# Optimization experiments

Hardware: AMD Instinct MI355X
Metric: run time of the kernel (lower is better)

Reference implementation:

```python
import jax, jax.numpy as jnp
import numpy as np

N_NODES = 50000
N_EDGES = 800000
D_IN = 64
D_OUT = 64


def setup_inputs() -> dict:
    key = jax.random.key(0)
    k1, k2, k3, k4 = jax.random.split(key, 4)
    x = jax.random.normal(k1, (N_NODES, D_IN), dtype=jnp.float32)
    edge_index = jax.random.randint(k2, (2, N_EDGES), 0, N_NODES, dtype=jnp.int64)
    W = jax.random.normal(k3, (D_IN, D_OUT), dtype=jnp.float32) * (1.0 / np.sqrt(D_IN))
    b = jax.random.normal(k4, (D_OUT,), dtype=jnp.float32) * 0.01
    return {"x": x, "edge_index": edge_index, "W": W, "b": b}


def reference(x, edge_index, W, b):
    N = x.shape[0]
    # Add self-loops (PyG GCNConv default add_self_loops=True)
    loop = jnp.arange(N, dtype=edge_index.dtype)
    src = jnp.concatenate([edge_index[0], loop])  # source j
    dst = jnp.concatenate([edge_index[1], loop])  # target i
    # Linear transform first (standard GCNConv: theta then propagate)
    xw = x @ W  # [N, D_OUT]
    # Symmetric degree normalization: deg over targets of (A + I)
    ones = jnp.ones(src.shape[0], dtype=x.dtype)
    deg = jax.ops.segment_sum(ones, dst, num_segments=N)
    dis = jnp.where(deg > 0, jax.lax.rsqrt(jnp.maximum(deg, 1.0)), 0.0)
    norm = dis[src] * dis[dst]  # [E+N]
    # Gather, weight, scatter-add
    msgs = norm[:, None] * xw[src]  # [E+N, D_OUT]
    out = jax.ops.segment_sum(msgs, dst, num_segments=N) + b
    return jax.nn.relu(out)
```

## Files before the change

kernel.cpp:

```cpp
#include <hip/hip_runtime.h>

#define N_NODES 50000
#define N_EDGES 800000
#define D 64
#define FINE_SHIFT 6
#define FINE_NODES 64
#define NBUCK ((N_NODES + FINE_NODES - 1) / FINE_NODES)
#define CAP 1280
#define EPB 4096
#define NPART ((N_EDGES + EPB - 1) / EPB)
#define GRPT (CAP / 256)

typedef _Float16 f16;
typedef __attribute__((ext_vector_type(2))) _Float16 f16x2;
typedef __attribute__((ext_vector_type(8))) _Float16 f16x8;
typedef __attribute__((ext_vector_type(4))) float f32x4;

__global__ __launch_bounds__(1024) void partition_edges(
    const int* __restrict__ src, const int* __restrict__ dst,
    int* __restrict__ cursor, unsigned int* __restrict__ binned,
    const float* __restrict__ W, f16* __restrict__ Wt16)
{
    __shared__ int hist[NBUCK];
    __shared__ int start_s[NBUCK];
    __shared__ int lcur[NBUCK];
    __shared__ int base_s[NBUCK];
    __shared__ unsigned int staged[EPB];

    int tid = threadIdx.x;
    int eb  = blockIdx.x * EPB;
    int total = N_EDGES - eb; if (total > EPB) total = EPB;

    if (blockIdx.x == 0) {
        for (int j = tid; j < 4096; j += 1024) {
            int n = j >> 6, k = j & 63;
            Wt16[j] = (f16)W[k * 64 + n];
        }
    }

    for (int i = tid; i < NBUCK; i += 1024) hist[i] = 0;
    __syncthreads();

    unsigned int rec[4];
    #pragma unroll
    for (int u = 0; u < 4; ++u) {
        int j = u * 1024 + tid;
        if (j < total) {
            unsigned int t = (unsigned int)dst[eb + j];
            rec[u] = (t << 16) | (unsigned int)src[eb + j];
            atomicAdd(&hist[t >> FINE_SHIFT], 1);
        } else rec[u] = 0xFFFFFFFFu;
    }
    __syncthreads();

    if (tid < 64) {
        int b0 = tid * 13;
        int v[13]; int run = 0;
        #pragma unroll
        for (int j = 0; j < 13; ++j) {
            int idx = b0 + j;
            int c = (idx < NBUCK) ? hist[idx] : 0;
            v[j] = run; run += c;
        }
        int s = run;
        #pragma unroll
        for (int off = 1; off < 64; off <<= 1) {
            int t = __shfl_up(s, off);
            if (tid >= off) s += t;
        }
        int excl = s - run;
        #pragma unroll
        for (int j = 0; j < 13; ++j) {
            int idx = b0 + j;
            if (idx < NBUCK) { start_s[idx] = excl + v[j]; lcur[idx] = excl + v[j]; }
        }
    }
    __syncthreads();

    for (int i = tid; i < NBUCK; i += 1024) {
        int c = hist[i];
        base_s[i] = c ? atomicAdd(&cursor[i], c) : 0;
    }
    #pragma unroll
    for (int u = 0; u < 4; ++u) {
        unsigned int v = rec[u];
        if (v != 0xFFFFFFFFu) {
            int cb = v >> (16 + FINE_SHIFT);
            int p  = atomicAdd(&lcur[cb], 1);
            staged[p] = v;
        }
    }
    __syncthreads();

    for (int i = tid; i < total; i += 1024) {
        unsigned int v = staged[i];
        int cb = v >> (16 + FINE_SHIFT);
        int gp = base_s[cb] + (i - start_s[cb]);
        if (gp < CAP) binned[(size_t)cb * CAP + gp] = v;
    }
}

__global__ __launch_bounds__(256) void xws_fused(
    const int* __restrict__ cursor, const unsigned int* __restrict__ binned,
    const float* __restrict__ x, const f16* __restrict__ Wt16,
    f16* __restrict__ xwsh)
{
    __shared__ f16 WtH[64][72];
    __shared__ f16 park[64][72];
    __shared__ int h[64];

    int bu = blockIdx.x, tid = threadIdx.x;
    int nb = bu * FINE_NODES;

    if (tid < 64) h[tid] = 0;
    __syncthreads();

    int cnt = cursor[bu]; if (cnt > CAP) cnt = CAP;
    const unsigned int* br = binned + (size_t)bu * CAP;
    for (int i = tid; i < cnt; i += 256)
        atomicAdd(&h[(br[i] >> 16) & 63], 1);

    for (int j = tid; j < 512; j += 256) {
        int row = j >> 3, seg = (j & 7) * 8;
        *(f16x8*)&WtH[row][seg] = *(const f16x8*)&Wt16[row * 64 + seg];
    }
    __syncthreads();

    int wave = tid >> 6, lane = tid & 63;
    int m = lane & 15, q = lane >> 4;

    int ar = nb + wave * 16 + m;
    if (ar >= N_NODES) ar = N_NODES - 1;
    const float4* x4 = (const float4*)x;
    size_t rb = (size_t)ar * 16;
    float4 p0 = x4[rb + q * 2];
    float4 p1 = x4[rb + q * 2 + 1];
    float4 p2 = x4[rb + 8 + q * 2];
    float4 p3 = x4[rb + 8 + q * 2 + 1];
    f16x8 a0 = { (f16)p0.x, (f16)p0.y, (f16)p0.z, (f16)p0.w,
                 (f16)p1.x, (f16)p1.y, (f16)p1.z, (f16)p1.w };
    f16x8 a1 = { (f16)p2.x, (f16)p2.y, (f16)p2.z, (f16)p2.w,
                 (f16)p3.x, (f16)p3.y, (f16)p3.z, (f16)p3.w };

    f32x4 acc[4];
    #pragma unroll
    for (int t = 0; t < 4; ++t) {
        int n0 = t * 16;
        f16x8 b0 = *(const f16x8*)&WtH[n0 + m][q * 8];
        f16x8 b1 = *(const f16x8*)&WtH[n0 + m][32 + q * 8];
        f32x4 z = { 0.f, 0.f, 0.f, 0.f };
        z = __builtin_amdgcn_mfma_f32_16x16x32_f16(a0, b0, z, 0, 0, 0);
        acc[t] = __builtin_amdgcn_mfma_f32_16x16x32_f16(a1, b1, z, 0, 0, 0);
    }

    float disr[4];
    #pragma unroll
    for (int r = 0; r < 4; ++r)
        disr[r] = rsqrtf((float)h[wave * 16 + q * 4 + r] + 1.0f);
    #pragma unroll
    for (int t = 0; t < 4; ++t) {
        int n0 = t * 16;
        #pragma unroll
        for (int r = 0; r < 4; ++r)
            park[wave * 16 + q * 4 + r][n0 + m] = (f16)(acc[t][r] * disr[r]);
    }
    __syncthreads();

    for (int j = tid; j < 512; j += 256) {
        int row = j >> 3, seg = (j & 7) * 8;
        if (nb + row < N_NODES)
            *(f16x8*)&xwsh[(size_t)(nb + row) * D + seg] = *(const f16x8*)&park[row][seg];
    }
}

__global__ __launch_bounds__(256) void gather_out(
    const int* __restrict__ cursor, const unsigned int* __restrict__ binned,
    const f16* __restrict__ xwsh, const float* __restrict__ b,
    float* __restrict__ out)
{
    __shared__ unsigned short ssrc[CAP];
    __shared__ int h[64], off_s[64], cur[64];

    int cb = blockIdx.x, tid = threadIdx.x;
    int wave = tid >> 6, lane = tid & 63;
    int nb = cb * FINE_NODES;
    int cnt = cursor[cb]; if (cnt > CAP) cnt = CAP;
    const unsigned int* br = binned + (size_t)cb * CAP;

    if (tid < 64) h[tid] = 0;
    __syncthreads();

    unsigned int rec[GRPT];
    #pragma unroll
    for (int u = 0; u < GRPT; ++u) {
        int j = u * 256 + tid;
        if (j < cnt) {
            rec[u] = br[j];
            atomicAdd(&h[(rec[u] >> 16) & 63], 1);
        } else rec[u] = 0xFFFFFFFFu;
    }
    __syncthreads();

    if (tid < 64) {
        int v = h[tid], s = v;
        #pragma unroll
        for (int off = 1; off < 64; off <<= 1) {
            int t = __shfl_up(s, off);
            if (tid >= off) s += t;
        }
        off_s[tid] = s - v;
        cur[tid]   = s - v;
    }
    __syncthreads();

    #pragma unroll
    for (int u = 0; u < GRPT; ++u) {
        unsigned int v = rec[u];
        if (v != 0xFFFFFFFFu) {
            int p = atomicAdd(&cur[(v >> 16) & 63], 1);
            ssrc[p] = (unsigned short)(v & 0xFFFFu);
        }
    }
    __syncthreads();

    const f16x2* xw2 = (const f16x2*)xwsh;
    float2* out2 = (float2*)out;
    int c32 = lane & 31;
    int hid = lane >> 5;
    float2 bl2 = ((const float2*)b)[c32];

    for (int i = 0; i < 16; ++i) {
        int nl = wave * 16 + i;
        int n  = nb + nl;
        if (n >= N_NODES) break;
        int off = off_s[nl], c = h[nl];
        float dn = rsqrtf((float)c + 1.0f);

        float2 acc; acc.x = 0.f; acc.y = 0.f;
        if (hid == 0) {
            f16x2 sv = xw2[(size_t)n * 32 + c32];
            acc.x = (float)sv.x; acc.y = (float)sv.y;
        }
        int k = off + hid, e = off + c;
        for (; k + 6 < e; k += 8) {
            int s0 = ssrc[k], s1 = ssrc[k + 2], s2 = ssrc[k + 4], s3 = ssrc[k + 6];
            f16x2 v0 = xw2[(size_t)s0 * 32 + c32];
            f16x2 v1 = xw2[(size_t)s1 * 32 + c32];
            f16x2 v2 = xw2[(size_t)s2 * 32 + c32];
            f16x2 v3 = xw2[(size_t)s3 * 32 + c32];
            acc.x += ((float)v0.x + (float)v1.x) + ((float)v2.x + (float)v3.x);
            acc.y += ((float)v0.y + (float)v1.y) + ((float)v2.y + (float)v3.y);
        }
        for (; k < e; k += 2) {
            f16x2 v = xw2[(size_t)ssrc[k] * 32 + c32];
            acc.x += (float)v.x; acc.y += (float)v.y;
        }
        acc.x += __shfl(acc.x, lane + 32);
        acc.y += __shfl(acc.y, lane + 32);
        if (hid == 0) {
            float2 r;
            r.x = fmaxf(bl2.x + dn * acc.x, 0.f);
            r.y = fmaxf(bl2.y + dn * acc.y, 0.f);
            out2[(size_t)n * 32 + c32] = r;
        }
    }
}

extern "C" void kernel_launch(void* const* d_in, const int* in_sizes, int n_in,
                              void* d_out, int out_size, void* d_ws, size_t ws_size,
                              hipStream_t stream) {
    const float* x  = (const float*)d_in[0];
    const int*   ei = (const int*)d_in[1];
    const float* W  = (const float*)d_in[2];
    const float* b  = (const float*)d_in[3];

    const int* src = ei;
    const int* dst = ei + N_EDGES;
    float* out = (float*)d_out;

    f16*          xwsh   = (f16*)d_ws;
    int*          cursor = (int*)(xwsh + (size_t)N_NODES * D);
    unsigned int* binned = (unsigned int*)(cursor + 784);
    f16*          Wt16   = (f16*)(binned + (size_t)NBUCK * CAP);

    hipMemsetAsync(cursor, 0, 784 * sizeof(int), stream);
    partition_edges<<<NPART, 1024, 0, stream>>>(src, dst, cursor, binned, W, Wt16);
    xws_fused<<<NBUCK, 256, 0, stream>>>(cursor, binned, x, Wt16, xwsh);
    gather_out<<<NBUCK, 256, 0, stream>>>(cursor, binned, xwsh, b, out);
}
```

Measured before the change: 120.5 us.

## Widen gather lanes, pad cursor atomics, vectorize edge partition loads

gather_out now runs 512 threads per block. Each node's edges are split across four 16-lane groups, each lane loading four fp16 channels, and the partial sums are reduced with xor shuffles. partition_edges handles 8192 edges per block, each thread reading 8 src/dst values with int4 loads, which halves the number of partition blocks. The per-bucket cursors are spaced 16 ints apart so global atomics from different buckets do not share cache lines. The trade-offs are more shuffle reduction work and larger blocks, which may reduce occupancy.

Result: faster. 109.6 us (-9.0%).

```diff
diff --git a/kernel.cpp b/kernel.cpp
--- a/kernel.cpp
+++ b/kernel.cpp
@@ -7,12 +7,12 @@
 #define FINE_NODES 64
 #define NBUCK ((N_NODES + FINE_NODES - 1) / FINE_NODES)
 #define CAP 1280
-#define EPB 4096
+#define EPB 8192
 #define NPART ((N_EDGES + EPB - 1) / EPB)
-#define GRPT (CAP / 256)
+#define CSTRIDE 16
 
 typedef _Float16 f16;
-typedef __attribute__((ext_vector_type(2))) _Float16 f16x2;
+typedef __attribute__((ext_vector_type(4))) _Float16 f16x4;
 typedef __attribute__((ext_vector_type(8))) _Float16 f16x8;
 typedef __attribute__((ext_vector_type(4))) float f32x4;
 
@@ -41,15 +41,27 @@
     for (int i = tid; i < NBUCK; i += 1024) hist[i] = 0;
     __syncthreads();
 
-    unsigned int rec[4];
-    #pragma unroll
-    for (int u = 0; u < 4; ++u) {
-        int j = u * 1024 + tid;
-        if (j < total) {
-            unsigned int t = (unsigned int)dst[eb + j];
-            rec[u] = (t << 16) | (unsigned int)src[eb + j];
-            atomicAdd(&hist[t >> FINE_SHIFT], 1);
-        } else rec[u] = 0xFFFFFFFFu;
+    unsigned int rec[8];
+    int jb = tid * 8;
+    if (jb < total) {
+        int4 s0 = *(const int4*)&src[eb + jb];
+        int4 s1 = *(const int4*)&src[eb + jb + 4];
+        int4 d0 = *(const int4*)&dst[eb + jb];
+        int4 d1 = *(const int4*)&dst[eb + jb + 4];
+        rec[0] = ((unsigned)d0.x << 16) | (unsigned)s0.x;
+        rec[1] = ((unsigned)d0.y << 16) | (unsigned)s0.y;
+        rec[2] = ((unsigned)d0.z << 16) | (unsigned)s0.z;
+        rec[3] = ((unsigned)d0.w << 16) | (unsigned)s0.w;
+        rec[4] = ((unsigned)d1.x << 16) | (unsigned)s1.x;
+        rec[5] = ((unsigned)d1.y << 16) | (unsigned)s1.y;
+        rec[6] = ((unsigned)d1.z << 16) | (unsigned)s1.z;
+        rec[7] = ((unsigned)d1.w << 16) | (unsigned)s1.w;
+        #pragma unroll
+        for (int u = 0; u < 8; ++u)
+            atomicAdd(&hist[rec[u] >> (16 + FINE_SHIFT)], 1);
+    } else {
+        #pragma unroll
+        for (int u = 0; u < 8; ++u) rec[u] = 0xFFFFFFFFu;
     }
     __syncthreads();
 
@@ -79,10 +91,10 @@
 
     for (int i = tid; i < NBUCK; i += 1024) {
         int c = hist[i];
-        base_s[i] = c ? atomicAdd(&cursor[i], c) : 0;
-    }
-    #pragma unroll
-    for (int u = 0; u < 4; ++u) {
+        base_s[i] = c ? atomicAdd(&cursor[i * CSTRIDE], c) : 0;
+    }
+    #pragma unroll
+    for (int u = 0; u < 8; ++u) {
         unsigned int v = rec[u];
         if (v != 0xFFFFFFFFu) {
             int cb = v >> (16 + FINE_SHIFT);
@@ -115,7 +127,7 @@
     if (tid < 64) h[tid] = 0;
     __syncthreads();
 
-    int cnt = cursor[bu]; if (cnt > CAP) cnt = CAP;
+    int cnt = cursor[bu * CSTRIDE]; if (cnt > CAP) cnt = CAP;
     const unsigned int* br = binned + (size_t)bu * CAP;
     for (int i = tid; i < cnt; i += 256)
         atomicAdd(&h[(br[i] >> 16) & 63], 1);
@@ -173,7 +185,7 @@
     }
 }
 
-__global__ __launch_bounds__(256) void gather_out(
+__global__ __launch_bounds__(512) void gather_out(
     const int* __restrict__ cursor, const unsigned int* __restrict__ binned,
     const f16* __restrict__ xwsh, const float* __restrict__ b,
     float* __restrict__ out)
@@ -184,16 +196,16 @@
     int cb = blockIdx.x, tid = threadIdx.x;
     int wave = tid >> 6, lane = tid & 63;
     int nb = cb * FINE_NODES;
-    int cnt = cursor[cb]; if (cnt > CAP) cnt = CAP;
+    int cnt = cursor[cb * CSTRIDE]; if (cnt > CAP) cnt = CAP;
     const unsigned int* br = binned + (size_t)cb * CAP;
 
     if (tid < 64) h[tid] = 0;
     __syncthreads();
 
-    unsigned int rec[GRPT];
-    #pragma unroll
-    for (int u = 0; u < GRPT; ++u) {
-        int j = u * 256 + tid;
+    unsigned int rec[3];
+    #pragma unroll
+    for (int u = 0; u < 3; ++u) {
+        int j = u * 512 + tid;
         if (j < cnt) {
             rec[u] = br[j];
             atomicAdd(&h[(rec[u] >> 16) & 63], 1);
@@ -214,7 +226,7 @@
     __syncthreads();
 
     #pragma unroll
-    for (int u = 0; u < GRPT; ++u) {
+    for (int u = 0; u < 3; ++u) {
         unsigned int v = rec[u];
         if (v != 0xFFFFFFFFu) {
             int p = atomicAdd(&cur[(v >> 16) & 63], 1);
@@ -223,45 +235,49 @@
     }
     __syncthreads();
 
-    const f16x2* xw2 = (const f16x2*)xwsh;
-    float2* out2 = (float2*)out;
-    int c32 = lane & 31;
-    int hid = lane >> 5;
-    float2 bl2 = ((const float2*)b)[c32];
-
-    for (int i = 0; i < 16; ++i) {
-        int nl = wave * 16 + i;
+    const f16x4* xw4 = (const f16x4*)xwsh;
+    const float4* b4p = (const float4*)b;
+    float4* out4 = (float4*)out;
+    int g = lane >> 4, c16 = lane & 15;
+
+    for (int i = 0; i < 8; ++i) {
+        int nl = wave * 8 + i;
         int n  = nb + nl;
         if (n >= N_NODES) break;
         int off = off_s[nl], c = h[nl];
-        float dn = rsqrtf((float)c + 1.0f);
-
-        float2 acc; acc.x = 0.f; acc.y = 0.f;
-        if (hid == 0) {
-            f16x2 sv = xw2[(size_t)n * 32 + c32];
-            acc.x = (float)sv.x; acc.y = (float)sv.y;
-        }
-        int k = off + hid, e = off + c;
-        for (; k + 6 < e; k += 8) {
-            int s0 = ssrc[k], s1 = ssrc[k + 2], s2 = ssrc[k + 4], s3 = ssrc[k + 6];
-            f16x2 v0 = xw2[(size_t)s0 * 32 + c32];
-            f16x2 v1 = xw2[(size_t)s1 * 32 + c32];
-            f16x2 v2 = xw2[(size_t)s2 * 32 + c32];
-            f16x2 v3 = xw2[(size_t)s3 * 32 + c32];
-            acc.x += ((float)v0.x + (float)v1.x) + ((float)v2.x + (float)v3.x);
-            acc.y += ((float)v0.y + (float)v1.y) + ((float)v2.y + (float)v3.y);
-        }
-        for (; k < e; k += 2) {
-            f16x2 v = xw2[(size_t)ssrc[k] * 32 + c32];
-            acc.x += (float)v.x; acc.y += (float)v.y;
-        }
-        acc.x += __shfl(acc.x, lane + 32);
-        acc.y += __shfl(acc.y, lane + 32);
-        if (hid == 0) {
-            float2 r;
-            r.x = fmaxf(bl2.x + dn * acc.x, 0.f);
-            r.y = fmaxf(bl2.y + dn * acc.y, 0.f);
-            out2[(size_t)n * 32 + c32] = r;
+
+        float a0 = 0.f, a1 = 0.f, a2 = 0.f, a3 = 0.f;
+        if (g == 0) {
+            f16x4 sv = xw4[(size_t)n * 16 + c16];
+            a0 = (float)sv.x; a1 = (float)sv.y; a2 = (float)sv.z; a3 = (float)sv.w;
+        }
+        int k = off + g, e = off + c;
+        for (; k + 4 < e; k += 8) {
+            int s0 = ssrc[k], s1 = ssrc[k + 4];
+            f16x4 v0 = xw4[(size_t)s0 * 16 + c16];
+            f16x4 v1 = xw4[(size_t)s1 * 16 + c16];
+            a0 += (float)v0.x + (float)v1.x;
+            a1 += (float)v0.y + (float)v1.y;
+            a2 += (float)v0.z + (float)v1.z;
+            a3 += (float)v0.w + (float)v1.w;
+        }
+        if (k < e) {
+            f16x4 v = xw4[(size_t)ssrc[k] * 16 + c16];
+            a0 += (float)v.x; a1 += (float)v.y; a2 += (float)v.z; a3 += (float)v.w;
+        }
+        a0 += __shfl_xor(a0, 32); a1 += __shfl_xor(a1, 32);
+        a2 += __shfl_xor(a2, 32); a3 += __shfl_xor(a3, 32);
+        a0 += __shfl_xor(a0, 16); a1 += __shfl_xor(a1, 16);
+        a2 += __shfl_xor(a2, 16); a3 += __shfl_xor(a3, 16);
+        if (g == 0) {
+            float dn = rsqrtf((float)c + 1.0f);
+            float4 bl = b4p[c16];
+            float4 r;
+            r.x = fmaxf(bl.x + dn * a0, 0.f);
+            r.y = fmaxf(bl.y + dn * a1, 0.f);
+            r.z = fmaxf(bl.z + dn * a2, 0.f);
+            r.w = fmaxf(bl.w + dn * a3, 0.f);
+            out4[(size_t)n * 16 + c16] = r;
         }
     }
 }
@@ -280,11 +296,11 @@
 
     f16*          xwsh   = (f16*)d_ws;
     int*          cursor = (int*)(xwsh + (size_t)N_NODES * D);
-    unsigned int* binned = (unsigned int*)(cursor + 784);
+    unsigned int* binned = (unsigned int*)(cursor + NBUCK * CSTRIDE);
     f16*          Wt16   = (f16*)(binned + (size_t)NBUCK * CAP);
 
-    hipMemsetAsync(cursor, 0, 784 * sizeof(int), stream);
+    hipMemsetAsync(cursor, 0, (size_t)NBUCK * CSTRIDE * sizeof(int), stream);
     partition_edges<<<NPART, 1024, 0, stream>>>(src, dst, cursor, binned, W, Wt16);
     xws_fused<<<NBUCK, 256, 0, stream>>>(cursor, binned, x, Wt16, xwsh);
-    gather_out<<<NBUCK, 256, 0, stream>>>(cursor, binned, xwsh, b, out);
+    gather_out<<<NBUCK, 512, 0, stream>>>(cursor, binned, xwsh, b, out);
 }
```
